# Kernel optimization log

Hardware: AMD Instinct MI355X
Metric: run time of the kernel (lower is better)

The kernel has to match this reference:

```python
import jax, jax.numpy as jnp
import numpy as np

T, B, XD, H, F = 1024, 256, 64, 256, 256  # seq_len, batch, x_dim, dim_RNN, feature dims
ALPHAS = [0.001, 0.01, 0.1]


def _alphas_per_unit():
    a = np.sort(np.asarray(ALPHAS, dtype=np.float32))
    assign = np.array([a[i % len(a)] for i in range(H)], dtype=np.float32)
    return jnp.asarray(np.sort(assign))  # [H]


def setup_inputs() -> dict:
    key = jax.random.key(0)
    ks = jax.random.split(key, 16)

    def w(k, shape, fan_in):
        return jax.random.normal(k, shape, jnp.float32) / np.sqrt(fan_in).astype(np.float32)

    return {
        "x": jax.random.normal(ks[0], (T, B, XD), jnp.float32),
        # feature_extractor_x: Linear(XD->F), Linear(F->F), tanh after each
        "Wx0": w(ks[1], (F, XD), XD), "bx0": jnp.zeros((F,), jnp.float32),
        "Wx1": w(ks[2], (F, F), F),   "bx1": jnp.zeros((F,), jnp.float32),
        # nn.RNN(F, H): tanh cell
        "Wih": w(ks[3], (H, F), F), "Whh": w(ks[4], (H, H), H),
        "bih": jnp.zeros((H,), jnp.float32), "bhh": jnp.zeros((H,), jnp.float32),
        # mlp_h_x: Linear(H->F), Linear(F->F), tanh after each
        "Wh0": w(ks[5], (F, H), H), "bh0": jnp.zeros((F,), jnp.float32),
        "Wh1": w(ks[6], (F, F), F), "bh1": jnp.zeros((F,), jnp.float32),
        # gen_out: Linear(F->XD)
        "Wg": w(ks[7], (XD, F), F), "bg": jnp.zeros((XD,), jnp.float32),
    }


def reference(x, Wx0, bx0, Wx1, bx1, Wih, Whh, bih, bhh, Wh0, bh0, Wh1, bh1, Wg, bg):
    act = jnp.tanh
    alphas = _alphas_per_unit()  # [H]

    # feature extractor applied to all timesteps at once (non-autonomous path)
    feat = act(jnp.einsum('tbx,fx->tbf', x, Wx0) + bx0)
    feat = act(jnp.einsum('tbf,gf->tbg', feat, Wx1) + bx1)  # [T,B,F]

    def step(h, ft):
        # y_t is generated from h BEFORE the recurrence update
        d = act(h @ Wh0.T + bh0)
        d = act(d @ Wh1.T + bh1)
        y = d @ Wg.T + bg  # [B,XD]
        h_raw = jnp.tanh(ft @ Wih.T + bih + h @ Whh.T + bhh)
        h_new = (1.0 - alphas) * h + alphas * h_raw  # leaky alpha-blend
        return h_new, y

    h0 = jnp.zeros((B, H), x.dtype)
    _, y = jax.lax.scan(step, h0, feat)  # y: [T,B,XD]
    return y
```

## Files before the change

### kernel.cpp

```cpp
#include <hip/hip_runtime.h>
#include <cstddef>


typedef _Float16 halfx8 __attribute__((ext_vector_type(8)));
typedef _Float16 halfx4 __attribute__((ext_vector_type(4)));
typedef float    f32x4  __attribute__((ext_vector_type(4)));

#define T_LEN 1024
#define B_SZ  256
#define H_DIM 256
#define M_ROWS (T_LEN * B_SZ)

__device__ __forceinline__ float fast_tanh(float x) {
  float e = __expf(2.0f * x);
  return 1.0f - 2.0f / (e + 1.0f);
}

__device__ __forceinline__ float alpha_of(int j) {
  return (j < 86) ? 0.001f : ((j < 171) ? 0.01f : 0.1f);
}

__device__ __forceinline__ void lds_barrier() {
  asm volatile("s_waitcnt lgkmcnt(0)\n\ts_barrier" ::: "memory");
}

template <int KCH, bool TANH, bool INF32, bool ZXT>
__global__ __launch_bounds__(512, 2)
void gemm8(const void* __restrict__ Ap, const float* __restrict__ W,
           const float* __restrict__ bias, void* __restrict__ Cp, int mtiles) {
  constexpr int K  = KCH * 32;
  constexpr int KP = K + 8;
  __shared__ __attribute__((aligned(16))) _Float16 Ah[32][KP];

  const int tid  = threadIdx.x;
  const int lane = tid & 63;
  const int wave = tid >> 6;
  const int l15  = lane & 15;
  const int quad = lane >> 4;
  const int jw   = wave * 32;

  halfx8 Bf[2][KCH];
  float  bcol[2];
  int    jj[2];
#pragma unroll
  for (int nt = 0; nt < 2; nt++) {
    jj[nt]   = jw + nt * 16 + l15;
    bcol[nt] = bias[jj[nt]];
#pragma unroll
    for (int ks = 0; ks < KCH; ks++) {
      const float* wp = W + (size_t)jj[nt] * K + ks * 32 + quad * 8;
      float4 w0 = *(const float4*)wp;
      float4 w1 = *(const float4*)(wp + 4);
      halfx8 f;
      f[0] = (_Float16)w0.x; f[1] = (_Float16)w0.y;
      f[2] = (_Float16)w0.z; f[3] = (_Float16)w0.w;
      f[4] = (_Float16)w1.x; f[5] = (_Float16)w1.y;
      f[6] = (_Float16)w1.z; f[7] = (_Float16)w1.w;
      Bf[nt][ks] = f;
    }
  }

  const int srow = tid >> 4;
  const int sk4  = tid & 15;

  for (int bm = blockIdx.x; bm < mtiles; bm += gridDim.x) {
    if constexpr (INF32) {
      const float* A = (const float*)Ap + (size_t)bm * 32 * K;
      constexpr int SEG = K / 64;
      float4 tv[SEG];
#pragma unroll
      for (int s = 0; s < SEG; s++)
        tv[s] = *(const float4*)(A + (size_t)srow * K + (sk4 + s * 16) * 4);
#pragma unroll
      for (int s = 0; s < SEG; s++) {
        halfx4 h;
        h[0] = (_Float16)tv[s].x; h[1] = (_Float16)tv[s].y;
        h[2] = (_Float16)tv[s].z; h[3] = (_Float16)tv[s].w;
        *(halfx4*)&Ah[srow][(sk4 + s * 16) * 4] = h;
      }
    } else {
      const _Float16* A = (const _Float16*)Ap + (size_t)bm * 32 * K;
      constexpr int SEG = K / 128;
      halfx8 tv[SEG];
#pragma unroll
      for (int s = 0; s < SEG; s++)
        tv[s] = *(const halfx8*)(A + (size_t)srow * K + (sk4 + s * 16) * 8);
#pragma unroll
      for (int s = 0; s < SEG; s++)
        *(halfx8*)&Ah[srow][(sk4 + s * 16) * 8] = tv[s];
    }
    lds_barrier();

    f32x4 acc[2][2];
#pragma unroll
    for (int mi = 0; mi < 2; mi++)
#pragma unroll
      for (int nt = 0; nt < 2; nt++) acc[mi][nt] = (f32x4){0.f, 0.f, 0.f, 0.f};

#pragma unroll
    for (int ks = 0; ks < KCH; ks++)
#pragma unroll
      for (int mi = 0; mi < 2; mi++) {
        halfx8 a = *(const halfx8*)&Ah[mi * 16 + l15][ks * 32 + quad * 8];
#pragma unroll
        for (int nt = 0; nt < 2; nt++)
          acc[mi][nt] = __builtin_amdgcn_mfma_f32_16x16x32_f16(a, Bf[nt][ks], acc[mi][nt], 0, 0, 0);
      }

    if constexpr (ZXT) {
      _Float16* C = (_Float16*)Cp;
      const size_t tb = (size_t)(bm >> 3) * (H_DIM * B_SZ) + (bm & 7) * 32 + quad * 4;
#pragma unroll
      for (int mi = 0; mi < 2; mi++)
#pragma unroll
        for (int nt = 0; nt < 2; nt++) {
          halfx4 o;
#pragma unroll
          for (int rg = 0; rg < 4; rg++)
            o[rg] = (_Float16)(acc[mi][nt][rg] + bcol[nt]);
          *(halfx4*)(C + tb + (size_t)jj[nt] * B_SZ + mi * 16) = o;
        }
    } else {
      _Float16* C = (_Float16*)Cp;
#pragma unroll
      for (int mi = 0; mi < 2; mi++)
#pragma unroll
        for (int nt = 0; nt < 2; nt++)
#pragma unroll
          for (int rg = 0; rg < 4; rg++) {
            const int rowg = bm * 32 + mi * 16 + quad * 4 + rg;
            float v = acc[mi][nt][rg] + bcol[nt];
            if (TANH) v = fast_tanh(v);
            C[(size_t)rowg * 256 + jj[nt]] = (_Float16)v;
          }
    }
    lds_barrier();
  }
}

__global__ __launch_bounds__(256, 2)
void gemm4_out(const _Float16* __restrict__ A, const float* __restrict__ W,
               const float* __restrict__ bias, float* __restrict__ C,
               int mtiles) {
  constexpr int K = 256, KCH = 8, KP = 264;
  __shared__ __attribute__((aligned(16))) _Float16 Ah[32][KP];

  const int tid  = threadIdx.x;
  const int lane = tid & 63;
  const int wave = tid >> 6;
  const int l15  = lane & 15;
  const int quad = lane >> 4;
  const int jcol = wave * 16 + l15;

  halfx8 Bf[KCH];
  const float bc = bias[jcol];
#pragma unroll
  for (int ks = 0; ks < KCH; ks++) {
    const float* wp = W + (size_t)jcol * K + ks * 32 + quad * 8;
    float4 w0 = *(const float4*)wp;
    float4 w1 = *(const float4*)(wp + 4);
    halfx8 f;
    f[0] = (_Float16)w0.x; f[1] = (_Float16)w0.y;
    f[2] = (_Float16)w0.z; f[3] = (_Float16)w0.w;
    f[4] = (_Float16)w1.x; f[5] = (_Float16)w1.y;
    f[6] = (_Float16)w1.z; f[7] = (_Float16)w1.w;
    Bf[ks] = f;
  }

  const int srow = tid >> 3;
  const int sk   = tid & 7;

  for (int bm = blockIdx.x; bm < mtiles; bm += gridDim.x) {
    const _Float16* Ab = A + (size_t)bm * 32 * K;
    halfx8 tv[4];
#pragma unroll
    for (int s = 0; s < 4; s++)
      tv[s] = *(const halfx8*)(Ab + (size_t)srow * K + (sk + s * 8) * 8);
#pragma unroll
    for (int s = 0; s < 4; s++)
      *(halfx8*)&Ah[srow][(sk + s * 8) * 8] = tv[s];
    lds_barrier();

    f32x4 acc[2];
#pragma unroll
    for (int mi = 0; mi < 2; mi++) acc[mi] = (f32x4){0.f, 0.f, 0.f, 0.f};
#pragma unroll
    for (int ks = 0; ks < KCH; ks++)
#pragma unroll
      for (int mi = 0; mi < 2; mi++) {
        halfx8 a = *(const halfx8*)&Ah[mi * 16 + l15][ks * 32 + quad * 8];
        acc[mi] = __builtin_amdgcn_mfma_f32_16x16x32_f16(a, Bf[ks], acc[mi], 0, 0, 0);
      }

#pragma unroll
    for (int mi = 0; mi < 2; mi++)
#pragma unroll
      for (int rg = 0; rg < 4; rg++) {
        const int rowg = bm * 32 + mi * 16 + quad * 4 + rg;
        C[(size_t)rowg * 64 + jcol] = acc[mi][rg] + bc;
      }
    lds_barrier();
  }
}

__global__ __launch_bounds__(512, 2)
void rnn_serial(const _Float16* __restrict__ zx,
                _Float16* __restrict__ h_all,
                const float* __restrict__ Whh,
                const float* __restrict__ bhh_p)
{
  __shared__ __attribute__((aligned(16))) _Float16 hB[2][16][264];

  const int tid  = threadIdx.x;
  const int lane = tid & 63;
  const int wave = tid >> 6;
  const int l15  = lane & 15;
  const int quad = lane >> 4;
  const int r0   = blockIdx.x * 16;
  const int jb   = wave * 32;

  halfx8 Af[2][8];
#pragma unroll
  for (int mt = 0; mt < 2; mt++) {
    const int j = jb + mt * 16 + l15;
#pragma unroll
    for (int ks = 0; ks < 8; ks++) {
      const float* wp = Whh + (size_t)j * H_DIM + ks * 32 + quad * 8;
      float4 w0 = *(const float4*)wp;
      float4 w1 = *(const float4*)(wp + 4);
      halfx8 f;
      f[0] = (_Float16)w0.x; f[1] = (_Float16)w0.y;
      f[2] = (_Float16)w0.z; f[3] = (_Float16)w0.w;
      f[4] = (_Float16)w1.x; f[5] = (_Float16)w1.y;
      f[6] = (_Float16)w1.z; f[7] = (_Float16)w1.w;
      Af[mt][ks] = f;
    }
  }

  float bj[2][4], aj[2][4], oma[2][4];
#pragma unroll
  for (int mt = 0; mt < 2; mt++)
#pragma unroll
    for (int rg = 0; rg < 4; rg++) {
      const int j = jb + mt * 16 + quad * 4 + rg;
      bj[mt][rg]  = bhh_p[j];
      aj[mt][rg]  = alpha_of(j);
      oma[mt][rg] = 1.0f - aj[mt][rg];
    }

  for (int i = tid; i < 16 * 264; i += 512) (&hB[0][0][0])[i] = (_Float16)0.0f;
  __syncthreads();

  const _Float16* rdp[2] = {&hB[0][l15][quad * 8], &hB[1][l15][quad * 8]};
  _Float16*       wrp[2] = {&hB[1][l15][jb + quad * 4], &hB[0][l15][jb + quad * 4]};

  constexpr int STRIDE = B_SZ * H_DIM;
  const _Float16* zp = zx    + (size_t)(r0 + l15) * H_DIM + jb + quad * 4;
  _Float16*       hp = h_all + (size_t)(r0 + l15) * H_DIM + jb + quad * 4;

  float  zc[2][4];
  halfx4 zA[2];
  {
#pragma unroll
    for (int mt = 0; mt < 2; mt++) {
      halfx4 z0 = *(const halfx4*)(zp + mt * 16);
      zA[mt]    = *(const halfx4*)(zp + mt * 16 + STRIDE);
#pragma unroll
      for (int rg = 0; rg < 4; rg++) zc[mt][rg] = (float)z0[rg];
    }
    zp += 2 * (size_t)STRIDE;
  }

  float  hreg[2][4];
  halfx4 hh4[2];
#pragma unroll
  for (int mt = 0; mt < 2; mt++) {
#pragma unroll
    for (int rg = 0; rg < 4; rg++) {
      hreg[mt][rg] = 0.0f;
      hh4[mt][rg]  = (_Float16)0.0f;
    }
  }

  auto step = [&](int p) {
    halfx4 znew[2];
#pragma unroll
    for (int mt = 0; mt < 2; mt++) znew[mt] = *(const halfx4*)(zp + mt * 16);
    zp += STRIDE;

    const _Float16* rd = rdp[p];
    halfx8 hb[8];
#pragma unroll
    for (int ks = 0; ks < 8; ks++) hb[ks] = *(const halfx8*)(rd + ks * 32);

    f32x4 acc[2];
#pragma unroll
    for (int mt = 0; mt < 2; mt++) acc[mt] = (f32x4){0.f, 0.f, 0.f, 0.f};
#pragma unroll
    for (int ks = 0; ks < 8; ks++)
#pragma unroll
      for (int mt = 0; mt < 2; mt++)
        acc[mt] = __builtin_amdgcn_mfma_f32_16x16x32_f16(Af[mt][ks], hb[ks], acc[mt], 0, 0, 0);

    _Float16* wr = wrp[p];
#pragma unroll
    for (int mt = 0; mt < 2; mt++) {
      halfx4 hnew;
#pragma unroll
      for (int rg = 0; rg < 4; rg++) {
        float hr = fast_tanh(zc[mt][rg] + acc[mt][rg] + bj[mt][rg]);
        float hn = oma[mt][rg] * hreg[mt][rg] + aj[mt][rg] * hr;
        hreg[mt][rg] = hn;
        hnew[rg] = (_Float16)hn;
      }
      *(halfx4*)(hp + mt * 16) = hh4[mt];
      hh4[mt] = hnew;
      *(halfx4*)(wr + mt * 16) = hnew;
    }
    hp += STRIDE;

    lds_barrier();

#pragma unroll
    for (int mt = 0; mt < 2; mt++) {
#pragma unroll
      for (int rg = 0; rg < 4; rg++) zc[mt][rg] = (float)zA[mt][rg];
      zA[mt] = znew[mt];
    }
  };

  for (int it = 0; it < T_LEN / 2; ++it) {
    step(0);
    step(1);
  }
}

extern "C" void kernel_launch(void* const* d_in, const int* in_sizes, int n_in,
                              void* d_out, int out_size, void* d_ws, size_t ws_size,
                              hipStream_t stream) {
  const float* x   = (const float*)d_in[0];
  const float* Wx0 = (const float*)d_in[1];
  const float* bx0 = (const float*)d_in[2];
  const float* Wx1 = (const float*)d_in[3];
  const float* bx1 = (const float*)d_in[4];
  const float* Wih = (const float*)d_in[5];
  const float* Whh = (const float*)d_in[6];
  const float* bih = (const float*)d_in[7];
  const float* bhh = (const float*)d_in[8];
  const float* Wh0 = (const float*)d_in[9];
  const float* bh0 = (const float*)d_in[10];
  const float* Wh1 = (const float*)d_in[11];
  const float* bh1 = (const float*)d_in[12];
  const float* Wg  = (const float*)d_in[13];
  const float* bg  = (const float*)d_in[14];
  float* out = (float*)d_out;

  _Float16* bufA = (_Float16*)d_ws;
  _Float16* bufB = bufA + (size_t)M_ROWS * 256;

  const int MT = M_ROWS / 32;

  gemm8<2, true, true, false><<<512, 512, 0, stream>>>(x, Wx0, bx0, bufA, MT);
  gemm8<8, true, false, false><<<512, 512, 0, stream>>>(bufA, Wx1, bx1, bufB, MT);
  gemm8<8, false, false, false><<<512, 512, 0, stream>>>(bufB, Wih, bih, bufA, MT);
  rnn_serial<<<16, 512, 0, stream>>>(bufA, bufB, Whh, bhh);
  gemm8<8, true, false, false><<<512, 512, 0, stream>>>(bufB, Wh0, bh0, bufA, MT);
  gemm8<8, true, false, false><<<512, 512, 0, stream>>>(bufA, Wh1, bh1, bufB, MT);
  gemm4_out<<<512, 256, 0, stream>>>(bufB, Wg, bg, out, MT);
}
```

Measured before the change: 1.460 ms.

## Fuse all stages into one persistent kernel overlapping RNN with GEMMs via flags

Replaces the seven-kernel pipeline with a prep kernel, which converts weights to fp16 once, and a single persistent mega kernel. Sixteen blocks run the serial RNN while 240 blocks first compute the feature MLP and input projection per tile, publishing per-tile ready flags. They then run the output MLP per tile as soon as the RNN progress counters say those timesteps are done. The aim is to hide the parallel GEMM work behind the serial recurrence and to keep intermediates in LDS instead of round-tripping through global memory. The cost is spin-wait polling and fences, and it depends on all 256 blocks being co-resident to avoid deadlock.

New measurement: 3.670 ms. +151.3%, slower.

```diff
diff --git a/kernel.cpp b/kernel.cpp
--- a/kernel.cpp
+++ b/kernel.cpp
@@ -10,6 +10,19 @@
 #define B_SZ  256
 #define H_DIM 256
 #define M_ROWS (T_LEN * B_SZ)
+#define MT     (M_ROWS / 32)
+#define NRB    16
+#define NGB    240
+
+__device__ _Float16 gWx0[256 * 64];
+__device__ _Float16 gWx1[256 * 256];
+__device__ _Float16 gWih[256 * 256];
+__device__ _Float16 gWh0[256 * 256];
+__device__ _Float16 gWh1[256 * 256];
+__device__ _Float16 gWg[64 * 256];
+__device__ float gBx0[256], gBx1[256], gBih[256], gBh0[256], gBh1[256], gBg[64];
+__device__ unsigned gZxFlag[MT];
+__device__ unsigned gProg[NRB];
 
 __device__ __forceinline__ float fast_tanh(float x) {
   float e = __expf(2.0f * x);
@@ -24,199 +37,173 @@
   asm volatile("s_waitcnt lgkmcnt(0)\n\ts_barrier" ::: "memory");
 }
 
-template <int KCH, bool TANH, bool INF32, bool ZXT>
-__global__ __launch_bounds__(512, 2)
-void gemm8(const void* __restrict__ Ap, const float* __restrict__ W,
-           const float* __restrict__ bias, void* __restrict__ Cp, int mtiles) {
-  constexpr int K  = KCH * 32;
-  constexpr int KP = K + 8;
-  __shared__ __attribute__((aligned(16))) _Float16 Ah[32][KP];
+__global__ void prep(const float* __restrict__ Wx0, const float* __restrict__ Wx1,
+                     const float* __restrict__ Wih, const float* __restrict__ Wh0,
+                     const float* __restrict__ Wh1, const float* __restrict__ Wg,
+                     const float* __restrict__ bx0, const float* __restrict__ bx1,
+                     const float* __restrict__ bih, const float* __restrict__ bh0,
+                     const float* __restrict__ bh1, const float* __restrict__ bg) {
+  const int i = blockIdx.x * blockDim.x + threadIdx.x;
+  if (i < MT) gZxFlag[i] = 0u;
+  if (i < NRB) gProg[i] = 0u;
+  if (i < 16384) { gWx0[i] = (_Float16)Wx0[i]; gWg[i] = (_Float16)Wg[i]; }
+  if (i < 65536) {
+    gWx1[i] = (_Float16)Wx1[i];
+    gWih[i] = (_Float16)Wih[i];
+    gWh0[i] = (_Float16)Wh0[i];
+    gWh1[i] = (_Float16)Wh1[i];
+  }
+  if (i < 256) {
+    gBx0[i] = bx0[i]; gBx1[i] = bx1[i]; gBih[i] = bih[i];
+    gBh0[i] = bh0[i]; gBh1[i] = bh1[i];
+  }
+  if (i < 64) gBg[i] = bg[i];
+}
+
+template <int KCH, bool TANH>
+__device__ __forceinline__ void stage_tile(const _Float16 (*__restrict__ Ah)[264],
+                                           _Float16 (*__restrict__ Ch)[264],
+                                           const _Float16* __restrict__ W,
+                                           const float* __restrict__ bias,
+                                           const int tid) {
+  constexpr int K = KCH * 32;
+  const int lane = tid & 63, wave = tid >> 6, l15 = lane & 15, quad = lane >> 4;
+  const int jw = wave * 32;
+
+  halfx8 Bf[2][KCH];
+  float bcol[2];
+  int jj[2];
+#pragma unroll
+  for (int nt = 0; nt < 2; nt++) {
+    jj[nt] = jw + nt * 16 + l15;
+    bcol[nt] = bias[jj[nt]];
+#pragma unroll
+    for (int ks = 0; ks < KCH; ks++)
+      Bf[nt][ks] = *(const halfx8*)(W + (size_t)jj[nt] * K + ks * 32 + quad * 8);
+  }
+
+  f32x4 acc[2][2];
+#pragma unroll
+  for (int mi = 0; mi < 2; mi++)
+#pragma unroll
+    for (int nt = 0; nt < 2; nt++) acc[mi][nt] = (f32x4){0.f, 0.f, 0.f, 0.f};
+
+#pragma unroll
+  for (int ks = 0; ks < KCH; ks++)
+#pragma unroll
+    for (int mi = 0; mi < 2; mi++) {
+      halfx8 a = *(const halfx8*)&Ah[mi * 16 + l15][ks * 32 + quad * 8];
+#pragma unroll
+      for (int nt = 0; nt < 2; nt++)
+        acc[mi][nt] = __builtin_amdgcn_mfma_f32_16x16x32_f16(a, Bf[nt][ks], acc[mi][nt], 0, 0, 0);
+    }
+
+#pragma unroll
+  for (int mi = 0; mi < 2; mi++)
+#pragma unroll
+    for (int nt = 0; nt < 2; nt++)
+#pragma unroll
+      for (int rg = 0; rg < 4; rg++) {
+        float v = acc[mi][nt][rg] + bcol[nt];
+        if (TANH) v = fast_tanh(v);
+        Ch[mi * 16 + quad * 4 + rg][jj[nt]] = (_Float16)v;
+      }
+}
+
+__device__ __forceinline__ void stage_zx(const _Float16 (*__restrict__ Ah)[264],
+                                         _Float16* __restrict__ C,
+                                         const _Float16* __restrict__ W,
+                                         const float* __restrict__ bias,
+                                         const int tid) {
+  constexpr int KCH = 8, K = 256;
+  const int lane = tid & 63, wave = tid >> 6, l15 = lane & 15, quad = lane >> 4;
+  const int jw = wave * 32;
+
+  halfx8 Bf[2][KCH];
+  float bcol[2];
+  int jj[2];
+#pragma unroll
+  for (int nt = 0; nt < 2; nt++) {
+    jj[nt] = jw + nt * 16 + l15;
+    bcol[nt] = bias[jj[nt]];
+#pragma unroll
+    for (int ks = 0; ks < KCH; ks++)
+      Bf[nt][ks] = *(const halfx8*)(W + (size_t)jj[nt] * K + ks * 32 + quad * 8);
+  }
+
+  f32x4 acc[2][2];
+#pragma unroll
+  for (int mi = 0; mi < 2; mi++)
+#pragma unroll
+    for (int nt = 0; nt < 2; nt++) acc[mi][nt] = (f32x4){0.f, 0.f, 0.f, 0.f};
+
+#pragma unroll
+  for (int ks = 0; ks < KCH; ks++)
+#pragma unroll
+    for (int mi = 0; mi < 2; mi++) {
+      halfx8 a = *(const halfx8*)&Ah[mi * 16 + l15][ks * 32 + quad * 8];
+#pragma unroll
+      for (int nt = 0; nt < 2; nt++)
+        acc[mi][nt] = __builtin_amdgcn_mfma_f32_16x16x32_f16(a, Bf[nt][ks], acc[mi][nt], 0, 0, 0);
+    }
+
+#pragma unroll
+  for (int mi = 0; mi < 2; mi++)
+#pragma unroll
+    for (int nt = 0; nt < 2; nt++)
+#pragma unroll
+      for (int rg = 0; rg < 4; rg++) {
+        const int row = mi * 16 + quad * 4 + rg;
+        C[(size_t)row * 256 + jj[nt]] = (_Float16)(acc[mi][nt][rg] + bcol[nt]);
+      }
+}
+
+__device__ __forceinline__ void stage_out(const _Float16 (*__restrict__ Ah)[264],
+                                          float* __restrict__ C,
+                                          const _Float16* __restrict__ W,
+                                          const float* __restrict__ bias,
+                                          const int tid) {
+  const int lane = tid & 63, wave = tid >> 6, l15 = lane & 15, quad = lane >> 4;
+  if (wave < 4) {
+    const int jcol = wave * 16 + l15;
+    halfx8 Bf[8];
+#pragma unroll
+    for (int ks = 0; ks < 8; ks++)
+      Bf[ks] = *(const halfx8*)(W + (size_t)jcol * 256 + ks * 32 + quad * 8);
+    const float bc = bias[jcol];
+    f32x4 acc[2];
+#pragma unroll
+    for (int mi = 0; mi < 2; mi++) acc[mi] = (f32x4){0.f, 0.f, 0.f, 0.f};
+#pragma unroll
+    for (int ks = 0; ks < 8; ks++)
+#pragma unroll
+      for (int mi = 0; mi < 2; mi++) {
+        halfx8 a = *(const halfx8*)&Ah[mi * 16 + l15][ks * 32 + quad * 8];
+        acc[mi] = __builtin_amdgcn_mfma_f32_16x16x32_f16(a, Bf[ks], acc[mi], 0, 0, 0);
+      }
+#pragma unroll
+    for (int mi = 0; mi < 2; mi++)
+#pragma unroll
+      for (int rg = 0; rg < 4; rg++)
+        C[(size_t)(mi * 16 + quad * 4 + rg) * 64 + jcol] = acc[mi][rg] + bc;
+  }
+}
+
+__device__ void rnn_block(const _Float16* __restrict__ zx,
+                          _Float16* __restrict__ h_all,
+                          const float* __restrict__ Whh,
+                          const float* __restrict__ bhh_p,
+                          _Float16 (*__restrict__ lds)[264],
+                          const int bid) {
+  _Float16(*hB)[16][264] = reinterpret_cast<_Float16(*)[16][264]>(&lds[0][0]);
 
   const int tid  = threadIdx.x;
   const int lane = tid & 63;
   const int wave = tid >> 6;
   const int l15  = lane & 15;
   const int quad = lane >> 4;
-  const int jw   = wave * 32;
-
-  halfx8 Bf[2][KCH];
-  float  bcol[2];
-  int    jj[2];
-#pragma unroll
-  for (int nt = 0; nt < 2; nt++) {
-    jj[nt]   = jw + nt * 16 + l15;
-    bcol[nt] = bias[jj[nt]];
-#pragma unroll
-    for (int ks = 0; ks < KCH; ks++) {
-      const float* wp = W + (size_t)jj[nt] * K + ks * 32 + quad * 8;
-      float4 w0 = *(const float4*)wp;
-      float4 w1 = *(const float4*)(wp + 4);
-      halfx8 f;
-      f[0] = (_Float16)w0.x; f[1] = (_Float16)w0.y;
-      f[2] = (_Float16)w0.z; f[3] = (_Float16)w0.w;
-      f[4] = (_Float16)w1.x; f[5] = (_Float16)w1.y;
-      f[6] = (_Float16)w1.z; f[7] = (_Float16)w1.w;
-      Bf[nt][ks] = f;
-    }
-  }
-
-  const int srow = tid >> 4;
-  const int sk4  = tid & 15;
-
-  for (int bm = blockIdx.x; bm < mtiles; bm += gridDim.x) {
-    if constexpr (INF32) {
-      const float* A = (const float*)Ap + (size_t)bm * 32 * K;
-      constexpr int SEG = K / 64;
-      float4 tv[SEG];
-#pragma unroll
-      for (int s = 0; s < SEG; s++)
-        tv[s] = *(const float4*)(A + (size_t)srow * K + (sk4 + s * 16) * 4);
-#pragma unroll
-      for (int s = 0; s < SEG; s++) {
-        halfx4 h;
-        h[0] = (_Float16)tv[s].x; h[1] = (_Float16)tv[s].y;
-        h[2] = (_Float16)tv[s].z; h[3] = (_Float16)tv[s].w;
-        *(halfx4*)&Ah[srow][(sk4 + s * 16) * 4] = h;
-      }
-    } else {
-      const _Float16* A = (const _Float16*)Ap + (size_t)bm * 32 * K;
-      constexpr int SEG = K / 128;
-      halfx8 tv[SEG];
-#pragma unroll
-      for (int s = 0; s < SEG; s++)
-        tv[s] = *(const halfx8*)(A + (size_t)srow * K + (sk4 + s * 16) * 8);
-#pragma unroll
-      for (int s = 0; s < SEG; s++)
-        *(halfx8*)&Ah[srow][(sk4 + s * 16) * 8] = tv[s];
-    }
-    lds_barrier();
-
-    f32x4 acc[2][2];
-#pragma unroll
-    for (int mi = 0; mi < 2; mi++)
-#pragma unroll
-      for (int nt = 0; nt < 2; nt++) acc[mi][nt] = (f32x4){0.f, 0.f, 0.f, 0.f};
-
-#pragma unroll
-    for (int ks = 0; ks < KCH; ks++)
-#pragma unroll
-      for (int mi = 0; mi < 2; mi++) {
-        halfx8 a = *(const halfx8*)&Ah[mi * 16 + l15][ks * 32 + quad * 8];
-#pragma unroll
-        for (int nt = 0; nt < 2; nt++)
-          acc[mi][nt] = __builtin_amdgcn_mfma_f32_16x16x32_f16(a, Bf[nt][ks], acc[mi][nt], 0, 0, 0);
-      }
-
-    if constexpr (ZXT) {
-      _Float16* C = (_Float16*)Cp;
-      const size_t tb = (size_t)(bm >> 3) * (H_DIM * B_SZ) + (bm & 7) * 32 + quad * 4;
-#pragma unroll
-      for (int mi = 0; mi < 2; mi++)
-#pragma unroll
-        for (int nt = 0; nt < 2; nt++) {
-          halfx4 o;
-#pragma unroll
-          for (int rg = 0; rg < 4; rg++)
-            o[rg] = (_Float16)(acc[mi][nt][rg] + bcol[nt]);
-          *(halfx4*)(C + tb + (size_t)jj[nt] * B_SZ + mi * 16) = o;
-        }
-    } else {
-      _Float16* C = (_Float16*)Cp;
-#pragma unroll
-      for (int mi = 0; mi < 2; mi++)
-#pragma unroll
-        for (int nt = 0; nt < 2; nt++)
-#pragma unroll
-          for (int rg = 0; rg < 4; rg++) {
-            const int rowg = bm * 32 + mi * 16 + quad * 4 + rg;
-            float v = acc[mi][nt][rg] + bcol[nt];
-            if (TANH) v = fast_tanh(v);
-            C[(size_t)rowg * 256 + jj[nt]] = (_Float16)v;
-          }
-    }
-    lds_barrier();
-  }
-}
-
-__global__ __launch_bounds__(256, 2)
-void gemm4_out(const _Float16* __restrict__ A, const float* __restrict__ W,
-               const float* __restrict__ bias, float* __restrict__ C,
-               int mtiles) {
-  constexpr int K = 256, KCH = 8, KP = 264;
-  __shared__ __attribute__((aligned(16))) _Float16 Ah[32][KP];
-
-  const int tid  = threadIdx.x;
-  const int lane = tid & 63;
-  const int wave = tid >> 6;
-  const int l15  = lane & 15;
-  const int quad = lane >> 4;
-  const int jcol = wave * 16 + l15;
-
-  halfx8 Bf[KCH];
-  const float bc = bias[jcol];
-#pragma unroll
-  for (int ks = 0; ks < KCH; ks++) {
-    const float* wp = W + (size_t)jcol * K + ks * 32 + quad * 8;
-    float4 w0 = *(const float4*)wp;
-    float4 w1 = *(const float4*)(wp + 4);
-    halfx8 f;
-    f[0] = (_Float16)w0.x; f[1] = (_Float16)w0.y;
-    f[2] = (_Float16)w0.z; f[3] = (_Float16)w0.w;
-    f[4] = (_Float16)w1.x; f[5] = (_Float16)w1.y;
-    f[6] = (_Float16)w1.z; f[7] = (_Float16)w1.w;
-    Bf[ks] = f;
-  }
-
-  const int srow = tid >> 3;
-  const int sk   = tid & 7;
-
-  for (int bm = blockIdx.x; bm < mtiles; bm += gridDim.x) {
-    const _Float16* Ab = A + (size_t)bm * 32 * K;
-    halfx8 tv[4];
-#pragma unroll
-    for (int s = 0; s < 4; s++)
-      tv[s] = *(const halfx8*)(Ab + (size_t)srow * K + (sk + s * 8) * 8);
-#pragma unroll
-    for (int s = 0; s < 4; s++)
-      *(halfx8*)&Ah[srow][(sk + s * 8) * 8] = tv[s];
-    lds_barrier();
-
-    f32x4 acc[2];
-#pragma unroll
-    for (int mi = 0; mi < 2; mi++) acc[mi] = (f32x4){0.f, 0.f, 0.f, 0.f};
-#pragma unroll
-    for (int ks = 0; ks < KCH; ks++)
-#pragma unroll
-      for (int mi = 0; mi < 2; mi++) {
-        halfx8 a = *(const halfx8*)&Ah[mi * 16 + l15][ks * 32 + quad * 8];
-        acc[mi] = __builtin_amdgcn_mfma_f32_16x16x32_f16(a, Bf[ks], acc[mi], 0, 0, 0);
-      }
-
-#pragma unroll
-    for (int mi = 0; mi < 2; mi++)
-#pragma unroll
-      for (int rg = 0; rg < 4; rg++) {
-        const int rowg = bm * 32 + mi * 16 + quad * 4 + rg;
-        C[(size_t)rowg * 64 + jcol] = acc[mi][rg] + bc;
-      }
-    lds_barrier();
-  }
-}
-
-__global__ __launch_bounds__(512, 2)
-void rnn_serial(const _Float16* __restrict__ zx,
-                _Float16* __restrict__ h_all,
-                const float* __restrict__ Whh,
-                const float* __restrict__ bhh_p)
-{
-  __shared__ __attribute__((aligned(16))) _Float16 hB[2][16][264];
-
-  const int tid  = threadIdx.x;
-  const int lane = tid & 63;
-  const int wave = tid >> 6;
-  const int l15  = lane & 15;
-  const int quad = lane >> 4;
-  const int r0   = blockIdx.x * 16;
+  const int r0   = bid * 16;
+  const int b2   = bid >> 1;
   const int jb   = wave * 32;
 
   halfx8 Af[2][8];
@@ -258,6 +245,26 @@
   const _Float16* zp = zx    + (size_t)(r0 + l15) * H_DIM + jb + quad * 4;
   _Float16*       hp = h_all + (size_t)(r0 + l15) * H_DIM + jb + quad * 4;
 
+  auto poll8 = [&](int tbase) {
+    bool ok = false;
+    while (!ok) {
+      ok = true;
+#pragma unroll
+      for (int i = 0; i < 8; i++) {
+        const int tt = tbase + i;
+        if (tt < T_LEN)
+          ok &= (__hip_atomic_load(&gZxFlag[tt * 8 + b2], __ATOMIC_RELAXED,
+                                   __HIP_MEMORY_SCOPE_AGENT) != 0u);
+      }
+      if (!ok) __builtin_amdgcn_s_sleep(2);
+    }
+    unsigned v = __hip_atomic_load(&gZxFlag[(tbase < T_LEN ? tbase : 0) * 8 + b2],
+                                   __ATOMIC_ACQUIRE, __HIP_MEMORY_SCOPE_AGENT);
+    asm volatile("" ::"v"(v));
+  };
+
+  poll8(0);
+
   float  zc[2][4];
   halfx4 zA[2];
   {
@@ -274,15 +281,11 @@
   float  hreg[2][4];
   halfx4 hh4[2];
 #pragma unroll
-  for (int mt = 0; mt < 2; mt++) {
-#pragma unroll
-    for (int rg = 0; rg < 4; rg++) {
-      hreg[mt][rg] = 0.0f;
-      hh4[mt][rg]  = (_Float16)0.0f;
-    }
-  }
-
-  auto step = [&](int p) {
+  for (int mt = 0; mt < 2; mt++)
+#pragma unroll
+    for (int rg = 0; rg < 4; rg++) { hreg[mt][rg] = 0.0f; hh4[mt][rg] = (_Float16)0.0f; }
+
+  auto step = [&](int p, bool pub, unsigned pval) {
     halfx4 znew[2];
 #pragma unroll
     for (int mt = 0; mt < 2; mt++) znew[mt] = *(const halfx4*)(zp + mt * 16);
@@ -319,7 +322,15 @@
     }
     hp += STRIDE;
 
-    lds_barrier();
+    if (pub) {
+      asm volatile("s_waitcnt vmcnt(0) lgkmcnt(0)\n\ts_barrier" ::: "memory");
+      if (tid == 0) {
+        __threadfence();
+        __hip_atomic_store(&gProg[bid], pval, __ATOMIC_RELEASE, __HIP_MEMORY_SCOPE_AGENT);
+      }
+    } else {
+      lds_barrier();
+    }
 
 #pragma unroll
     for (int mt = 0; mt < 2; mt++) {
@@ -330,8 +341,79 @@
   };
 
   for (int it = 0; it < T_LEN / 2; ++it) {
-    step(0);
-    step(1);
+    const int t0 = 2 * it;
+    if ((it & 3) == 0) poll8(t0 + 2);
+    step(0, false, 0u);
+    step(1, (it & 3) == 3, (unsigned)(t0 + 2));
+  }
+}
+
+__global__ __launch_bounds__(512, 1)
+void mega(const float* __restrict__ x, _Float16* __restrict__ bufA,
+          _Float16* __restrict__ bufB, float* __restrict__ out,
+          const float* __restrict__ Whh, const float* __restrict__ bhh_p) {
+  __shared__ __attribute__((aligned(16))) _Float16 lds[2][32][264];
+  const int tid = threadIdx.x;
+
+  if (blockIdx.x < NRB) {
+    rnn_block(bufA, bufB, Whh, bhh_p, lds[0], blockIdx.x);
+    return;
+  }
+
+  const int g = blockIdx.x - NRB;
+  _Float16(*Ah)[264] = lds[0];
+  _Float16(*Bh)[264] = lds[1];
+
+  for (int bm = g; bm < MT; bm += NGB) {
+    {
+      const int srow = tid >> 4, sk4 = tid & 15;
+      float4 tv = *(const float4*)(x + (size_t)(bm * 32 + srow) * 64 + sk4 * 4);
+      halfx4 h;
+      h[0] = (_Float16)tv.x; h[1] = (_Float16)tv.y;
+      h[2] = (_Float16)tv.z; h[3] = (_Float16)tv.w;
+      *(halfx4*)&Ah[srow][sk4 * 4] = h;
+    }
+    lds_barrier();
+    stage_tile<2, true>(Ah, Bh, gWx0, gBx0, tid);
+    lds_barrier();
+    stage_tile<8, true>(Bh, Ah, gWx1, gBx1, tid);
+    lds_barrier();
+    stage_zx(Ah, bufA + (size_t)bm * 32 * 256, gWih, gBih, tid);
+    __syncthreads();
+    if (tid == 0) {
+      __threadfence();
+      __hip_atomic_store(&gZxFlag[bm], 1u, __ATOMIC_RELEASE, __HIP_MEMORY_SCOPE_AGENT);
+    }
+    __syncthreads();
+  }
+
+  for (int bm = g; bm < MT; bm += NGB) {
+    const int t = bm >> 3, b2 = bm & 7;
+    const unsigned need = (unsigned)(t + 1);
+    if (tid == 0) {
+      while (__hip_atomic_load(&gProg[2 * b2], __ATOMIC_ACQUIRE,
+                               __HIP_MEMORY_SCOPE_AGENT) < need)
+        __builtin_amdgcn_s_sleep(8);
+      while (__hip_atomic_load(&gProg[2 * b2 + 1], __ATOMIC_ACQUIRE,
+                               __HIP_MEMORY_SCOPE_AGENT) < need)
+        __builtin_amdgcn_s_sleep(8);
+    }
+    __syncthreads();
+    {
+      const int srow = tid >> 4, sk4 = tid & 15;
+      const _Float16* hsrc = bufB + (size_t)bm * 32 * 256 + (size_t)srow * 256 + sk4 * 16;
+      halfx8 t0 = *(const halfx8*)hsrc;
+      halfx8 t1 = *(const halfx8*)(hsrc + 8);
+      *(halfx8*)&Ah[srow][sk4 * 16] = t0;
+      *(halfx8*)&Ah[srow][sk4 * 16 + 8] = t1;
+    }
+    lds_barrier();
+    stage_tile<8, true>(Ah, Bh, gWh0, gBh0, tid);
+    lds_barrier();
+    stage_tile<8, true>(Bh, Ah, gWh1, gBh1, tid);
+    lds_barrier();
+    stage_out(Ah, out + (size_t)bm * 32 * 64, gWg, gBg, tid);
+    lds_barrier();
   }
 }
 
@@ -358,13 +440,7 @@
   _Float16* bufA = (_Float16*)d_ws;
   _Float16* bufB = bufA + (size_t)M_ROWS * 256;
 
-  const int MT = M_ROWS / 32;
-
-  gemm8<2, true, true, false><<<512, 512, 0, stream>>>(x, Wx0, bx0, bufA, MT);
-  gemm8<8, true, false, false><<<512, 512, 0, stream>>>(bufA, Wx1, bx1, bufB, MT);
-  gemm8<8, false, false, false><<<512, 512, 0, stream>>>(bufB, Wih, bih, bufA, MT);
-  rnn_serial<<<16, 512, 0, stream>>>(bufA, bufB, Whh, bhh);
-  gemm8<8, true, false, false><<<512, 512, 0, stream>>>(bufB, Wh0, bh0, bufA, MT);
-  gemm8<8, true, false, false><<<512, 512, 0, stream>>>(bufA, Wh1, bh1, bufB, MT);
-  gemm4_out<<<512, 256, 0, stream>>>(bufB, Wg, bg, out, MT);
-}
+  prep<<<256, 256, 0, stream>>>(Wx0, Wx1, Wih, Wh0, Wh1, Wg,
+                                bx0, bx1, bih, bh0, bh1, bg);
+  mega<<<NRB + NGB, 512, 0, stream>>>(x, bufA, bufB, out, Whh, bhh);
+}
```
